# Kernel tuning notes

Measured on AMD Instinct MI355X. Metric: run time of the kernel, lower is better.

The kernel has to match this reference:

```python
import jax, jax.numpy as jnp
import numpy as np

B, N, D, Y = 4, 2048, 512, 8921


def setup_inputs() -> dict:
    key = jax.random.key(0)
    ks = jax.random.split(key, 9)
    scale = 1.0 / np.sqrt(D)
    return {
        "x": jax.random.normal(ks[0], (B, N, D), jnp.float32),
        "target": (jax.random.uniform(ks[1], (B, Y), jnp.float32) > 0.98).astype(jnp.float32),
        "y_flow": jax.random.normal(ks[2], (B, Y), jnp.float32),
        "U_w": jax.random.normal(ks[3], (Y, D), jnp.float32) * scale,
        "Ug_w": jax.random.normal(ks[4], (Y, D), jnp.float32) * scale,
        "final_w": jax.random.normal(ks[5], (Y, D), jnp.float32) * scale,
        "final_b": jax.random.normal(ks[6], (Y,), jnp.float32) * scale,
        "gate_w": jax.random.normal(ks[7], (D,), jnp.float32) * scale,
        "gate_b": jax.random.normal(ks[8], (), jnp.float32) * scale,
    }


def reference(x, target, y_flow, U_w, Ug_w, final_w, final_b, gate_w, gate_b):
    # Label attention branch: alpha = softmax(U_w @ x^T) over tokens -> [B, Y, N]
    alpha = jax.nn.softmax(jnp.einsum("yd,bnd->byn", U_w, x), axis=-1)
    m = jnp.einsum("byn,bnd->byd", alpha, x)  # [B, Y, D]

    # Gate attention branch
    alpha_g = jax.nn.softmax(jnp.einsum("yd,bnd->byn", Ug_w, x), axis=-1)
    m_g = jnp.einsum("byn,bnd->byd", alpha_g, x)  # [B, Y, D]

    # gate = tanh(Linear(D,1)(m_gate)) -> [B, Y]
    gate = jnp.tanh(jnp.einsum("byd,d->by", m_g, gate_w) + gate_b)

    # y = sum_d(final_w * m) + final_b + y_flow * gate
    y = jnp.einsum("yd,byd->by", final_w, m) + final_b + y_flow * gate

    # BCEWithLogitsLoss (mean): logaddexp(0, y) - y * target, numerically stable
    loss = jnp.mean(jnp.logaddexp(0.0, y) - y * target)
    return (y, loss)
```

## Files before the change

kernel.cpp:

```cpp
#include <hip/hip_runtime.h>
#include <stdint.h>

#define BQ 4
#define NQ 2048
#define DQ 512
#define YQ 8921
#define YGRP 140
#define NH 4
#define NCHQ 32
#define NUNITS (YGRP * BQ * NH)
#define NLP 140
#define GXOFF 65536
#define L2E 1.44269504088896340736f

typedef __attribute__((ext_vector_type(8))) short bf16x8;
typedef __attribute__((ext_vector_type(4))) float f32x4;

__device__ inline short f2bf(float f) {
  unsigned u = __float_as_uint(f);
  u += 0x7fffu + ((u >> 16) & 1u);
  return (short)(u >> 16);
}

__device__ inline bf16x8 pack8(float4 a, float4 b) {
  bf16x8 h;
  h[0] = f2bf(a.x); h[1] = f2bf(a.y); h[2] = f2bf(a.z); h[3] = f2bf(a.w);
  h[4] = f2bf(b.x); h[5] = f2bf(b.y); h[6] = f2bf(b.z); h[7] = f2bf(b.w);
  return h;
}

__device__ inline void gl_lds16(const void* g, void* l) {
  __builtin_amdgcn_global_load_lds((const __attribute__((address_space(1))) void*)g,
                                   (__attribute__((address_space(3))) void*)l, 16, 0, 0);
}

__global__ __launch_bounds__(256) void prep_gx(const float* __restrict__ x,
                                               const float* __restrict__ gate_w,
                                               float* __restrict__ gx) {
  int rid = blockIdx.x * 4 + (threadIdx.x >> 6);
  int lane = threadIdx.x & 63;
  const float* src = x + (size_t)rid * DQ + lane * 8;
  float4 v0 = *(const float4*)src;
  float4 v1 = *(const float4*)(src + 4);
  const float* gwp = gate_w + lane * 8;
  float s = v0.x * gwp[0] + v0.y * gwp[1] + v0.z * gwp[2] + v0.w * gwp[3]
          + v1.x * gwp[4] + v1.y * gwp[5] + v1.z * gwp[6] + v1.w * gwp[7];
#pragma unroll
  for (int d = 1; d < 64; d <<= 1) s += __shfl_xor(s, d);
  if (lane == 0) gx[rid] = s;
}

__global__ __launch_bounds__(256) void prep_xfrag(const float* __restrict__ x,
                                                  char* __restrict__ ws_x2) {
  __shared__ float xs[16 * 512];
  int t = blockIdx.x;
  const float* src = x + ((size_t)t << 13);
  int tid = threadIdx.x;
#pragma unroll
  for (int i = 0; i < 8; ++i)
    *(float4*)(xs + i * 1024 + tid * 4) = *(const float4*)(src + i * 1024 + tid * 4);
  __syncthreads();
  char* dst = ws_x2 + ((size_t)t << 14);
#pragma unroll
  for (int i = 0; i < 4; ++i) {
    int s = i * 256 + tid;
    int l = s & 63, kk = s >> 6;
    int row = l & 15, g = l >> 4;
    const float* p = xs + row * 512 + kk * 32 + g * 8;
    *(bf16x8*)(dst + s * 16) = pack8(*(const float4*)p, *(const float4*)(p + 4));
  }
}

__global__ __launch_bounds__(256) void prep_w(const float* __restrict__ Uw,
                                              const float* __restrict__ Gw,
                                              const float* __restrict__ Fw,
                                              char* __restrict__ ws_w) {
  int rid = blockIdx.x * 4 + (threadIdx.x >> 6);
  if (rid >= 3 * YQ) return;
  int lane = threadIdx.x & 63;
  int mat = rid / YQ, y = rid % YQ;
  const float* src = (mat == 0 ? Uw : (mat == 1 ? Gw : Fw)) + (size_t)y * DQ + lane * 8;
  *(bf16x8*)(ws_w + (size_t)rid * 1024 + lane * 16) =
      pack8(*(const float4*)src, *(const float4*)(src + 4));
}

template<bool FULL>
__global__ __launch_bounds__(256, 2) void fused_kernel(
    const float* __restrict__ x, const char* __restrict__ ws_x2,
    const char* __restrict__ ws_w,
    const float* __restrict__ Uw, const float* __restrict__ Gw,
    const float* __restrict__ Fw, const float* __restrict__ gx,
    float4* __restrict__ ws_state) {
  extern __shared__ char smem[];
  const int tid = threadIdx.x, l = tid & 63, w = tid >> 6;
  const int lr = l & 15, lg4 = l >> 4;
  int u = (blockIdx.x & 7) * (NUNITS / 8) + (blockIdx.x >> 3);
  const int b = u / (YGRP * NH);
  const int r0 = u % (YGRP * NH);
  const int yg = r0 / NH, nh = r0 % NH;
  const int ybase = yg * 64 + w * 16;
  const int nbase = nh * (NQ / NH);

  bf16x8 wU[16], wG[16], wF[16];
  {
    int y = ybase + lr; if (y >= YQ) y = YQ - 1;
    if constexpr (FULL) {
      const char* p0 = ws_w + ((size_t)y * DQ + lg4 * 8) * 2;
#pragma unroll
      for (int kk = 0; kk < 16; ++kk) {
        wU[kk] = *(const bf16x8*)(p0 + kk * 64);
        wG[kk] = *(const bf16x8*)(p0 + (size_t)YQ * 1024 + kk * 64);
        wF[kk] = *(const bf16x8*)(p0 + (size_t)YQ * 2048 + kk * 64);
      }
    } else {
      const float* pu = Uw + (size_t)y * DQ + lg4 * 8;
      const float* pg = Gw + (size_t)y * DQ + lg4 * 8;
      const float* pf = Fw + (size_t)y * DQ + lg4 * 8;
#pragma unroll
      for (int kk = 0; kk < 16; ++kk) {
        wU[kk] = pack8(*(const float4*)(pu + kk * 32), *(const float4*)(pu + kk * 32 + 4));
        wG[kk] = pack8(*(const float4*)(pg + kk * 32), *(const float4*)(pg + kk * 32 + 4));
        wF[kk] = pack8(*(const float4*)(pf + kk * 32), *(const float4*)(pf + kk * 32 + 4));
      }
    }
  }

  float lU = 0.f, aU = 0.f, lG = 0.f, aG = 0.f;

  if constexpr (FULL) {
    *(float2*)(smem + GXOFF + tid * 8) = *(const float2*)(gx + b * NQ + nbase + tid * 2);
    const char* xb = ws_x2 + (((size_t)(b * 128 + nh * 32)) << 14);
    auto stage = [&](int c) {
      const char* src = xb + ((size_t)c << 14);
      char* lb = smem + (c & 3) * 16384;
#pragma unroll
      for (int j = 0; j < 4; ++j) {
        int s = w * 4 + j;
        gl_lds16(src + s * 1024 + l * 16, lb + s * 1024);
      }
    };
    auto compute = [&](int c) {
      const char* ab = smem + (c & 3) * 16384 + l * 16;
      f32x4 sU = {0.f, 0.f, 0.f, 0.f}, sG = sU, sF = sU;
      __builtin_amdgcn_s_setprio(1);
#pragma unroll
      for (int kk = 0; kk < 16; ++kk) {
        bf16x8 a = *(const bf16x8*)(ab + kk * 1024);
        sU = __builtin_amdgcn_mfma_f32_16x16x32_bf16(a, wU[kk], sU, 0, 0, 0);
        sG = __builtin_amdgcn_mfma_f32_16x16x32_bf16(a, wG[kk], sG, 0, 0, 0);
        sF = __builtin_amdgcn_mfma_f32_16x16x32_bf16(a, wF[kk], sF, 0, 0, 0);
      }
      __builtin_amdgcn_s_setprio(0);
      float4 gxv = *(const float4*)(smem + GXOFF + c * 64 + lg4 * 16);
      float gv[4] = {gxv.x, gxv.y, gxv.z, gxv.w};
#pragma unroll
      for (int r = 0; r < 4; ++r) {
        float eu = __builtin_amdgcn_exp2f(sU[r] * L2E);
        lU += eu; aU = fmaf(eu, sF[r], aU);
        float eg = __builtin_amdgcn_exp2f(sG[r] * L2E);
        lG += eg; aG = fmaf(eg, gv[r], aG);
      }
    };

    __syncthreads();
    stage(0); stage(1);
    asm volatile("s_waitcnt vmcnt(4)" ::: "memory");
    __builtin_amdgcn_s_barrier();

#pragma unroll 1
    for (int cp = 0; cp < NCHQ / 2; ++cp) {
      const int c0 = 2 * cp;
      if (cp < NCHQ / 2 - 1) { stage(c0 + 2); stage(c0 + 3); }
      compute(c0);
      if (cp < NCHQ / 2 - 1) asm volatile("s_waitcnt vmcnt(8)" ::: "memory");
      else                   asm volatile("s_waitcnt vmcnt(0)" ::: "memory");
      compute(c0 + 1);
      if (cp < NCHQ / 2 - 1) {
        asm volatile("s_waitcnt vmcnt(4)" ::: "memory");
        __builtin_amdgcn_sched_barrier(0);
        __builtin_amdgcn_s_barrier();
      }
    }
  } else {
    const float* gxb = gx + b * NQ + nbase + lg4 * 4;
    for (int c = 0; c < NCHQ; ++c) {
      __syncthreads();
#pragma unroll
      for (int j = 0; j < 4; ++j) {
        int slot = j * 256 + tid;
        int kk = slot >> 6, l2 = slot & 63;
        int row = l2 & 15, g4 = l2 >> 4;
        const float* g = x + ((size_t)(b * NQ + nbase + c * 16 + row)) * DQ
                       + kk * 32 + g4 * 8;
        *(bf16x8*)(smem + slot * 16) = pack8(*(const float4*)g, *(const float4*)(g + 4));
      }
      __syncthreads();
      const char* ab = smem + l * 16;
      f32x4 sU = {0.f, 0.f, 0.f, 0.f}, sG = sU, sF = sU;
#pragma unroll
      for (int kk = 0; kk < 16; ++kk) {
        bf16x8 a = *(const bf16x8*)(ab + kk * 1024);
        sU = __builtin_amdgcn_mfma_f32_16x16x32_bf16(a, wU[kk], sU, 0, 0, 0);
        sG = __builtin_amdgcn_mfma_f32_16x16x32_bf16(a, wG[kk], sG, 0, 0, 0);
        sF = __builtin_amdgcn_mfma_f32_16x16x32_bf16(a, wF[kk], sF, 0, 0, 0);
      }
      float4 gxv = *(const float4*)(gxb + c * 16);
      float gv[4] = {gxv.x, gxv.y, gxv.z, gxv.w};
#pragma unroll
      for (int r = 0; r < 4; ++r) {
        float eu = __builtin_amdgcn_exp2f(sU[r] * L2E);
        lU += eu; aU = fmaf(eu, sF[r], aU);
        float eg = __builtin_amdgcn_exp2f(sG[r] * L2E);
        lG += eg; aG = fmaf(eg, gv[r], aG);
      }
    }
  }

#pragma unroll
  for (int d = 16; d < 64; d <<= 1) {
    lU += __shfl_xor(lU, d); aU += __shfl_xor(aU, d);
    lG += __shfl_xor(lG, d); aG += __shfl_xor(aG, d);
  }

  int y = ybase + lr;
  if (lg4 == 0 && y < YQ) {
    float4 st; st.x = lU; st.y = aU; st.z = lG; st.w = aG;
    ws_state[(size_t)(b * NH + nh) * YQ + y] = st;
  }
}

__global__ __launch_bounds__(256) void merge_kernel(
    const float4* __restrict__ ws_state, const float* __restrict__ fb,
    const float* __restrict__ gate_b, const float* __restrict__ yflow,
    const float* __restrict__ target, float* __restrict__ out_y,
    float* __restrict__ loss_part) {
  __shared__ float sb[256];
  int t = blockIdx.x * 256 + threadIdx.x;
  float lt = 0.f;
  if (t < BQ * YQ) {
    int b = t / YQ, y = t % YQ;
    float lU = 0.f, aU = 0.f, lG = 0.f, aG = 0.f;
#pragma unroll
    for (int nh = 0; nh < NH; ++nh) {
      float4 s = ws_state[(size_t)(b * NH + nh) * YQ + y];
      lU += s.x; aU += s.y; lG += s.z; aG += s.w;
    }
    float gate = tanhf(aG / lG + gate_b[0]);
    float yv = aU / lU + fb[y] + yflow[t] * gate;
    out_y[t] = yv;
    float tg = target[t];
    lt = fmaxf(yv, 0.f) + log1pf(__expf(-fabsf(yv))) - yv * tg;
  }
  sb[threadIdx.x] = lt;
  __syncthreads();
  for (int st = 128; st > 0; st >>= 1) {
    if (threadIdx.x < st) sb[threadIdx.x] += sb[threadIdx.x + st];
    __syncthreads();
  }
  if (threadIdx.x == 0) loss_part[blockIdx.x] = sb[0];
}

__global__ __launch_bounds__(256) void loss_kernel(const float* __restrict__ lp,
                                                   float* __restrict__ out) {
  __shared__ float sb[256];
  float s = (threadIdx.x < NLP) ? lp[threadIdx.x] : 0.f;
  sb[threadIdx.x] = s;
  __syncthreads();
  for (int st = 128; st > 0; st >>= 1) {
    if (threadIdx.x < st) sb[threadIdx.x] += sb[threadIdx.x + st];
    __syncthreads();
  }
  if (threadIdx.x == 0) out[BQ * YQ] = sb[0] / (float)(BQ * YQ);
}

extern "C" void kernel_launch(void* const* d_in, const int* in_sizes, int n_in,
                              void* d_out, int out_size, void* d_ws, size_t ws_size,
                              hipStream_t stream) {
  const float* x      = (const float*)d_in[0];
  const float* target = (const float*)d_in[1];
  const float* yflow  = (const float*)d_in[2];
  const float* Uw     = (const float*)d_in[3];
  const float* Gw     = (const float*)d_in[4];
  const float* Fw     = (const float*)d_in[5];
  const float* fb     = (const float*)d_in[6];
  const float* gw     = (const float*)d_in[7];
  const float* gb     = (const float*)d_in[8];
  float* out = (float*)d_out;
  char* ws = (char*)d_ws;

  const size_t xbytes  = (size_t)BQ * NQ * DQ * 2;
  const size_t wbytes  = (size_t)3 * YQ * DQ * 2;
  const size_t gxbytes = (size_t)BQ * NQ * 4;
  const size_t stbytes = (size_t)BQ * NH * YQ * 16;
  const size_t lpbytes = (size_t)NLP * 4;
  const bool full = ws_size >= xbytes + wbytes + gxbytes + stbytes + lpbytes;

  char* ws_x2; char* ws_w; float* gxp; float4* stp; float* lp;
  if (full) {
    ws_x2 = ws; ws_w = ws + xbytes;
    gxp = (float*)(ws + xbytes + wbytes);
    stp = (float4*)(ws + xbytes + wbytes + gxbytes);
    lp  = (float*)(ws + xbytes + wbytes + gxbytes + stbytes);
  } else {
    ws_x2 = nullptr; ws_w = nullptr;
    gxp = (float*)ws;
    stp = (float4*)(ws + gxbytes);
    lp  = (float*)(ws + gxbytes + stbytes);
  }

  (void)hipFuncSetAttribute(reinterpret_cast<const void*>(&fused_kernel<true>),
                            hipFuncAttributeMaxDynamicSharedMemorySize, 67584);
  (void)hipFuncSetAttribute(reinterpret_cast<const void*>(&fused_kernel<false>),
                            hipFuncAttributeMaxDynamicSharedMemorySize, 16384);

  prep_gx<<<dim3(2048), 256, 0, stream>>>(x, gw, gxp);
  if (full) {
    prep_xfrag<<<dim3(BQ * 128), 256, 0, stream>>>(x, ws_x2);
    prep_w<<<dim3((3 * YQ + 3) / 4), 256, 0, stream>>>(Uw, Gw, Fw, ws_w);
    fused_kernel<true ><<<dim3(NUNITS), 256, 67584, stream>>>(
        x, ws_x2, ws_w, Uw, Gw, Fw, gxp, stp);
  } else {
    fused_kernel<false><<<dim3(NUNITS), 256, 16384, stream>>>(
        x, ws_x2, ws_w, Uw, Gw, Fw, gxp, stp);
  }
  merge_kernel<<<dim3(NLP), 256, 0, stream>>>(stp, fb, gb, yflow, target, out, lp);
  loss_kernel<<<1, 256, 0, stream>>>(lp, out);
}
```

Baseline: 217.6 us.

## Software-pipeline MFMA and softmax tail; fold gate projection into x prep

The fused loop is restructured so the MFMA block for the next chunk is issued before the exp/accumulate tail of the previous chunk, with a barrier per chunk instead of per pair. This lets transcendental and VALU work overlap matrix-core work, at the cost of holding a second set of accumulators (more VGPR pressure, which could hurt 2-waves-per-SIMD occupancy). Separately, the x·gate_w dot product is computed inside prep_xfrag from the already-staged shared tile, which removes the separate prep_gx launch and its second read of x.

```diff
diff --git a/kernel.cpp b/kernel.cpp
--- a/kernel.cpp
+++ b/kernel.cpp
@@ -51,7 +51,9 @@
 }
 
 __global__ __launch_bounds__(256) void prep_xfrag(const float* __restrict__ x,
-                                                  char* __restrict__ ws_x2) {
+                                                  const float* __restrict__ gate_w,
+                                                  char* __restrict__ ws_x2,
+                                                  float* __restrict__ gx) {
   __shared__ float xs[16 * 512];
   int t = blockIdx.x;
   const float* src = x + ((size_t)t << 13);
@@ -69,6 +71,19 @@
     const float* p = xs + row * 512 + kk * 32 + g * 8;
     *(bf16x8*)(dst + s * 16) = pack8(*(const float4*)p, *(const float4*)(p + 4));
   }
+  int row = tid >> 4, sub = tid & 15;
+  const float* xr = xs + row * 512 + sub * 32;
+  const float* gw = gate_w + sub * 32;
+  float s = 0.f;
+#pragma unroll
+  for (int i = 0; i < 8; ++i) {
+    float4 a = *(const float4*)(xr + i * 4);
+    float4 g = *(const float4*)(gw + i * 4);
+    s += a.x * g.x + a.y * g.y + a.z * g.z + a.w * g.w;
+  }
+  s += __shfl_xor(s, 1); s += __shfl_xor(s, 2);
+  s += __shfl_xor(s, 4); s += __shfl_xor(s, 8);
+  if (sub == 0) gx[t * 16 + row] = s;
 }
 
 __global__ __launch_bounds__(256) void prep_w(const float* __restrict__ Uw,
@@ -139,9 +154,10 @@
         gl_lds16(src + s * 1024 + l * 16, lb + s * 1024);
       }
     };
-    auto compute = [&](int c) {
+    auto mfma_only = [&](int c, f32x4& sU, f32x4& sG, f32x4& sF) {
       const char* ab = smem + (c & 3) * 16384 + l * 16;
-      f32x4 sU = {0.f, 0.f, 0.f, 0.f}, sG = sU, sF = sU;
+#pragma unroll
+      for (int r = 0; r < 4; ++r) { sU[r] = 0.f; sG[r] = 0.f; sF[r] = 0.f; }
       __builtin_amdgcn_s_setprio(1);
 #pragma unroll
       for (int kk = 0; kk < 16; ++kk) {
@@ -151,6 +167,8 @@
         sF = __builtin_amdgcn_mfma_f32_16x16x32_bf16(a, wF[kk], sF, 0, 0, 0);
       }
       __builtin_amdgcn_s_setprio(0);
+    };
+    auto tail = [&](int c, const f32x4& sU, const f32x4& sG, const f32x4& sF) {
       float4 gxv = *(const float4*)(smem + GXOFF + c * 64 + lg4 * 16);
       float gv[4] = {gxv.x, gxv.y, gxv.z, gxv.w};
 #pragma unroll
@@ -167,20 +185,30 @@
     asm volatile("s_waitcnt vmcnt(4)" ::: "memory");
     __builtin_amdgcn_s_barrier();
 
+    f32x4 pU, pG, pF, qU, qG, qF;
+    mfma_only(0, pU, pG, pF);
+
 #pragma unroll 1
-    for (int cp = 0; cp < NCHQ / 2; ++cp) {
+    for (int cp = 0; cp < 15; ++cp) {
       const int c0 = 2 * cp;
-      if (cp < NCHQ / 2 - 1) { stage(c0 + 2); stage(c0 + 3); }
-      compute(c0);
-      if (cp < NCHQ / 2 - 1) asm volatile("s_waitcnt vmcnt(8)" ::: "memory");
-      else                   asm volatile("s_waitcnt vmcnt(0)" ::: "memory");
-      compute(c0 + 1);
-      if (cp < NCHQ / 2 - 1) {
-        asm volatile("s_waitcnt vmcnt(4)" ::: "memory");
-        __builtin_amdgcn_sched_barrier(0);
-        __builtin_amdgcn_s_barrier();
-      }
+      stage(c0 + 2); stage(c0 + 3);
+      asm volatile("s_waitcnt vmcnt(8)" ::: "memory");
+      __builtin_amdgcn_sched_barrier(0);
+      __builtin_amdgcn_s_barrier();
+      mfma_only(c0 + 1, qU, qG, qF);
+      tail(c0, pU, pG, pF);
+      asm volatile("s_waitcnt vmcnt(4)" ::: "memory");
+      __builtin_amdgcn_sched_barrier(0);
+      __builtin_amdgcn_s_barrier();
+      mfma_only(c0 + 2, pU, pG, pF);
+      tail(c0 + 1, qU, qG, qF);
     }
+    asm volatile("s_waitcnt vmcnt(0)" ::: "memory");
+    __builtin_amdgcn_sched_barrier(0);
+    __builtin_amdgcn_s_barrier();
+    mfma_only(31, qU, qG, qF);
+    tail(30, pU, pG, pF);
+    tail(31, qU, qG, qF);
   } else {
     const float* gxb = gx + b * NQ + nbase + lg4 * 4;
     for (int c = 0; c < NCHQ; ++c) {
@@ -313,13 +341,13 @@
   (void)hipFuncSetAttribute(reinterpret_cast<const void*>(&fused_kernel<false>),
                             hipFuncAttributeMaxDynamicSharedMemorySize, 16384);
 
-  prep_gx<<<dim3(2048), 256, 0, stream>>>(x, gw, gxp);
   if (full) {
-    prep_xfrag<<<dim3(BQ * 128), 256, 0, stream>>>(x, ws_x2);
+    prep_xfrag<<<dim3(BQ * 128), 256, 0, stream>>>(x, gw, ws_x2, gxp);
     prep_w<<<dim3((3 * YQ + 3) / 4), 256, 0, stream>>>(Uw, Gw, Fw, ws_w);
     fused_kernel<true ><<<dim3(NUNITS), 256, 67584, stream>>>(
         x, ws_x2, ws_w, Uw, Gw, Fw, gxp, stp);
   } else {
+    prep_gx<<<dim3(2048), 256, 0, stream>>>(x, gw, gxp);
     fused_kernel<false><<<dim3(NUNITS), 256, 16384, stream>>>(
         x, ws_x2, ws_w, Uw, Gw, Fw, gxp, stp);
   }
```

Measured after the change: 219.7 us. Within noise of the previous version (+1.0%).
